# Kernel optimization log

Hardware: AMD Instinct MI355X
Metric: run time of the kernel (lower is better)

The kernel has to match this reference:

```python
import jax, jax.numpy as jnp
import numpy as np
from jax.scipy.special import logsumexp

E = 512      # input_size (= 2*hidden_size)
T = 24       # output_size (num CRF tags)
B, S = 32, 512
HEADS = 2


def setup_inputs() -> dict:
    key = jax.random.key(0)
    ks = jax.random.split(key, 12)
    u = lambda k, shape, a: jax.random.uniform(k, shape, jnp.float32, -a, a)
    inp = {
        "encoder_outputs": jax.random.normal(ks[0], (B, S, E), jnp.float32),
        "labels": jax.random.randint(ks[1], (B, S), 0, T),
        "mask": jnp.ones((B, S), dtype=bool),
        # nn.MultiheadAttention params
        "Win": u(ks[2], (3 * E, E), E ** -0.5),
        "bin_": jnp.zeros((3 * E,), jnp.float32),
        "Wout": u(ks[3], (E, E), E ** -0.5),
        "bout": jnp.zeros((E,), jnp.float32),
        # crf_linear
        "crf_w": u(ks[4], (T, E), E ** -0.5),
        "crf_b": u(ks[5], (T,), E ** -0.5),
        # torchcrf CRF params (uniform(-0.1, 0.1))
        "start_t": u(ks[6], (T,), 0.1),
        "end_t": u(ks[7], (T,), 0.1),
        "trans": u(ks[8], (T, T), 0.1),
        # entity_linear
        "ent_w": u(ks[9], (2, E), E ** -0.5),
        "ent_b": u(ks[10], (2,), E ** -0.5),
    }
    return inp


def _mha(x, Win, bin_, Wout, bout):
    b, s, e = x.shape
    hd = e // HEADS
    qkv = x @ Win.T + bin_                       # [B,S,3E]
    q, k, v = jnp.split(qkv, 3, axis=-1)
    q = q.reshape(b, s, HEADS, hd)
    k = k.reshape(b, s, HEADS, hd)
    v = v.reshape(b, s, HEADS, hd)
    scores = jnp.einsum("bqhd,bkhd->bhqk", q, k) / jnp.sqrt(jnp.float32(hd))
    attn = jax.nn.softmax(scores, axis=-1)       # [B,H,S,S]
    out = jnp.einsum("bhqk,bkhd->bqhd", attn, v).reshape(b, s, e)
    return out @ Wout.T + bout


def _crf_numerator(em, labels, maskf, start_t, end_t, trans):
    # em: [B,S,T] emissions, labels: [B,S] int, maskf: [B,S] float (mask[:,0]==1)
    bidx = jnp.arange(em.shape[0])
    score = start_t[labels[:, 0]] + em[bidx, 0, labels[:, 0]]
    prev, cur = labels[:, :-1], labels[:, 1:]
    em_t = jnp.take_along_axis(em[:, 1:], cur[:, :, None], axis=2)[..., 0]
    score = score + ((trans[prev, cur] + em_t) * maskf[:, 1:]).sum(axis=1)
    seq_ends = maskf.sum(axis=1).astype(jnp.int32) - 1
    last_tags = labels[bidx, seq_ends]
    return score + end_t[last_tags]


def _crf_normalizer(em, maskf, start_t, end_t, trans):
    score0 = start_t + em[:, 0]                  # [B,T]

    def step(score, x):
        e_t, m_t = x                             # [B,T], [B]
        nxt = logsumexp(score[:, :, None] + trans[None] + e_t[:, None, :], axis=1)
        return jnp.where(m_t[:, None] > 0, nxt, score), None

    xs = (em[:, 1:].swapaxes(0, 1), maskf[:, 1:].T)
    score, _ = jax.lax.scan(step, score0, xs)
    return logsumexp(score + end_t, axis=1)


def _viterbi(em, start_t, end_t, trans):
    # decode is called without a mask -> mask of all ones
    score0 = start_t + em[:, 0]                  # [B,T]

    def step(score, e_t):
        nxt = score[:, :, None] + trans[None] + e_t[:, None, :]  # [B,T,T]
        return nxt.max(axis=1), nxt.argmax(axis=1)

    score, history = jax.lax.scan(step, score0, em[:, 1:].swapaxes(0, 1))
    last = jnp.argmax(score + end_t, axis=1)     # [B]

    def back(tag, hist):
        prev = jnp.take_along_axis(hist, tag[:, None], axis=1)[:, 0]
        return prev, prev

    _, prevs = jax.lax.scan(back, last, history, reverse=True)  # [S-1,B]
    return jnp.concatenate([prevs, last[None]], axis=0).T       # [B,S]


def reference(encoder_outputs, labels, mask, Win, bin_, Wout, bout,
              crf_w, crf_b, start_t, end_t, trans, ent_w, ent_b):
    attn = _mha(encoder_outputs, Win, bin_, Wout, bout)
    dec = jax.nn.relu(attn)                      # [B,S,E]
    fc_out = dec @ crf_w.T + crf_b               # [B,S,T]
    maskf = mask.astype(fc_out.dtype)
    num = _crf_numerator(fc_out, labels, maskf, start_t, end_t, trans)
    den = _crf_normalizer(fc_out, maskf, start_t, end_t, trans)
    llh = (num - den).sum() / maskf.sum()        # reduction='token_mean'
    crf_out = _viterbi(fc_out, start_t, end_t, trans)
    seg_out = jax.nn.log_softmax(dec @ ent_w.T + ent_b, axis=2)
    return crf_out, seg_out, -llh
```

## Files before the change

### kernel.cpp

```cpp
#include <hip/hip_runtime.h>

#define BB 32
#define SS 512
#define EE 512
#define NHH 2
#define HDD 256
#define E3 1536
#define NT 24
#define MR (BB*SS)

#define WAVE_BAR() __builtin_amdgcn_wave_barrier()

typedef _Float16 half8  __attribute__((ext_vector_type(8)));
typedef _Float16 half4v __attribute__((ext_vector_type(4)));
typedef float    f32x4  __attribute__((ext_vector_type(4)));

template<int BN>
__global__ __launch_bounds__(256) void mfma_gemm(
    const float* __restrict__ A, int lda, long sAhi, long sAlo, int zA,
    const float* __restrict__ B, int ldb, long sBhi, long sBlo, int zB,
    const float* __restrict__ bias,
    float* __restrict__ C, int ldc, long sChi, long sClo, int zC,
    int K, int relu)
{
    __shared__ __align__(16) _Float16 sAh[8*640];
    __shared__ __align__(16) _Float16 sAl[8*640];
    __shared__ __align__(16) _Float16 sBh[8*640];
    __shared__ __align__(16) _Float16 sBl[8*640];

    const int t = threadIdx.x;
    const int z = blockIdx.z;
    const int za = zA + z, zb = zB + z, zc = zC + z;
    const float* Ab = A + (size_t)(za>>1)*sAhi + (size_t)(za&1)*sAlo
                        + (size_t)blockIdx.y*128*lda;
    const float* Bb = B + (size_t)(zb>>1)*sBhi + (size_t)(zb&1)*sBlo
                        + (BN ? (size_t)blockIdx.x*128
                              : (size_t)blockIdx.x*128*ldb);

    const int wv = t >> 6, lane = t & 63;
    const int wm = wv >> 1, wn = wv & 1;
    const int lm = lane & 15, lq = lane >> 4;

    f32x4 acc[4][4];
#pragma unroll
    for (int i = 0; i < 4; ++i)
#pragma unroll
        for (int j = 0; j < 4; ++j) acc[i][j] = (f32x4){0.f,0.f,0.f,0.f};

    const int r8  = t >> 3;
    const int kc  = (t & 7) * 4;
    const int bnk = (t >> 7) * 16;
    const int bnn = t & 127;

    for (int k0 = 0; k0 < K; k0 += 32) {
        float4 ga[4], gb[4]; float gv[16];
#pragma unroll
        for (int i = 0; i < 4; ++i)
            ga[i] = *(const float4*)(Ab + (size_t)(r8 + 32*i)*lda + k0 + kc);
        if (BN) {
#pragma unroll
            for (int i = 0; i < 16; ++i)
                gv[i] = Bb[(size_t)(k0 + bnk + i)*ldb + bnn];
        } else {
#pragma unroll
            for (int i = 0; i < 4; ++i)
                gb[i] = *(const float4*)(Bb + (size_t)(r8 + 32*i)*ldb + k0 + kc);
        }
        __syncthreads();
#pragma unroll
        for (int i = 0; i < 4; ++i) {
            const int row  = r8 + 32*i;
            const int base = (row >> 4)*640 + (row & 15)*40 + kc;
            float4 a = ga[i];
            _Float16 h0 = (_Float16)a.x, h1 = (_Float16)a.y,
                     h2 = (_Float16)a.z, h3 = (_Float16)a.w;
            _Float16 l0 = (_Float16)(a.x - (float)h0),
                     l1 = (_Float16)(a.y - (float)h1),
                     l2 = (_Float16)(a.z - (float)h2),
                     l3 = (_Float16)(a.w - (float)h3);
            *(half4v*)&sAh[base] = (half4v){h0,h1,h2,h3};
            *(half4v*)&sAl[base] = (half4v){l0,l1,l2,l3};
        }
        if (BN) {
#pragma unroll
            for (int i = 0; i < 16; ++i) {
                const int k = bnk + i;
                float v = gv[i];
                _Float16 h = (_Float16)v;
                _Float16 l = (_Float16)(v - (float)h);
                const int base = (bnn >> 4)*640 + (bnn & 15)*40 + k;
                sBh[base] = h;
                sBl[base] = l;
            }
        } else {
#pragma unroll
            for (int i = 0; i < 4; ++i) {
                const int row  = r8 + 32*i;
                const int base = (row >> 4)*640 + (row & 15)*40 + kc;
                float4 b = gb[i];
                _Float16 h0 = (_Float16)b.x, h1 = (_Float16)b.y,
                         h2 = (_Float16)b.z, h3 = (_Float16)b.w;
                _Float16 l0 = (_Float16)(b.x - (float)h0),
                         l1 = (_Float16)(b.y - (float)h1),
                         l2 = (_Float16)(b.z - (float)h2),
                         l3 = (_Float16)(b.w - (float)h3);
                *(half4v*)&sBh[base] = (half4v){h0,h1,h2,h3};
                *(half4v*)&sBl[base] = (half4v){l0,l1,l2,l3};
            }
        }
        __syncthreads();

        half8 bhf[4], blf[4];
#pragma unroll
        for (int j = 0; j < 4; ++j) {
            const int tb = (wn*4 + j)*640 + lm*40 + lq*8;
            bhf[j] = *(const half8*)&sBh[tb];
            blf[j] = *(const half8*)&sBl[tb];
        }
#pragma unroll
        for (int i = 0; i < 4; ++i) {
            const int ta = (wm*4 + i)*640 + lm*40 + lq*8;
            half8 ah = *(const half8*)&sAh[ta];
            half8 al = *(const half8*)&sAl[ta];
#pragma unroll
            for (int j = 0; j < 4; ++j) {
                acc[i][j] = __builtin_amdgcn_mfma_f32_16x16x32_f16(ah, bhf[j], acc[i][j], 0, 0, 0);
                acc[i][j] = __builtin_amdgcn_mfma_f32_16x16x32_f16(al, bhf[j], acc[i][j], 0, 0, 0);
                acc[i][j] = __builtin_amdgcn_mfma_f32_16x16x32_f16(ah, blf[j], acc[i][j], 0, 0, 0);
            }
        }
    }

    float* Cb = C + (size_t)(zc>>1)*sChi + (size_t)(zc&1)*sClo;
#pragma unroll
    for (int j = 0; j < 4; ++j) {
        const int col = blockIdx.x*128 + (wn*4 + j)*16 + lm;
        const float bj = bias ? bias[col] : 0.f;
#pragma unroll
        for (int i = 0; i < 4; ++i) {
            const int row0 = blockIdx.y*128 + (wm*4 + i)*16 + lq*4;
#pragma unroll
            for (int r = 0; r < 4; ++r) {
                float v = acc[i][j][r] + bj;
                if (relu) v = fmaxf(v, 0.f);
                Cb[(size_t)(row0 + r)*ldc + col] = v;
            }
        }
    }
}

__global__ __launch_bounds__(256) void softmax_rows(float* __restrict__ scores)
{
    const int w    = threadIdx.x >> 6;
    const int lane = threadIdx.x & 63;
    const size_t row = (size_t)blockIdx.x * 4 + w;
    float* p = scores + row * SS + lane * 8;
    float4 v0 = *(float4*)(p);
    float4 v1 = *(float4*)(p + 4);
    const float scale = 0.0625f;
    float m = fmaxf(fmaxf(fmaxf(v0.x, v0.y), fmaxf(v0.z, v0.w)),
                    fmaxf(fmaxf(v1.x, v1.y), fmaxf(v1.z, v1.w)));
#pragma unroll
    for (int off = 32; off >= 1; off >>= 1) m = fmaxf(m, __shfl_xor(m, off));
    v0.x = __expf((v0.x - m) * scale); v0.y = __expf((v0.y - m) * scale);
    v0.z = __expf((v0.z - m) * scale); v0.w = __expf((v0.w - m) * scale);
    v1.x = __expf((v1.x - m) * scale); v1.y = __expf((v1.y - m) * scale);
    v1.z = __expf((v1.z - m) * scale); v1.w = __expf((v1.w - m) * scale);
    float sum = v0.x + v0.y + v0.z + v0.w + v1.x + v1.y + v1.z + v1.w;
#pragma unroll
    for (int off = 32; off >= 1; off >>= 1) sum += __shfl_xor(sum, off);
    float inv = 1.f / sum;
    v0.x *= inv; v0.y *= inv; v0.z *= inv; v0.w *= inv;
    v1.x *= inv; v1.y *= inv; v1.z *= inv; v1.w *= inv;
    *(float4*)(p)     = v0;
    *(float4*)(p + 4) = v1;
}

__global__ __launch_bounds__(192) void fc_crf_kernel(
    const float* __restrict__ dec, const float* __restrict__ W,
    const float* __restrict__ bias, float* __restrict__ out)
{
    __shared__ __align__(16) float Ws[NT][516];
    for (int i = threadIdx.x; i < NT*128; i += 192) {
        int j = i >> 7, c = (i & 127) * 4;
        *(float4*)&Ws[j][c] = *(const float4*)(W + (size_t)j*EE + c);
    }
    __syncthreads();
    const int t = threadIdx.x;
    const int rloc = t / NT;
    const int j = t - rloc * NT;
    const int row = blockIdx.x * 8 + rloc;
    const float4* a = (const float4*)(dec + (size_t)row * EE);
    float acc = 0.f;
#pragma unroll 4
    for (int i = 0; i < 128; ++i) {
        float4 x = a[i];
        float4 y = *(const float4*)&Ws[j][i*4];
        acc += x.x*y.x + x.y*y.y + x.z*y.z + x.w*y.w;
    }
    out[(size_t)row * NT + j] = acc + bias[j];
}

__global__ __launch_bounds__(256) void crf_seg_kernel(
    const float* __restrict__ fc, const int* __restrict__ labels,
    const float* __restrict__ start_t, const float* __restrict__ end_t,
    const float* __restrict__ trans, const float* __restrict__ dec,
    const float* __restrict__ ent_w, const float* __restrict__ ent_b,
    float* __restrict__ num, float* __restrict__ den,
    float* __restrict__ crf_out, float* __restrict__ segout)
{
    __shared__ unsigned char hist[4][(SS-1)*NT];

    const int blk = blockIdx.x;
    if (blk >= 24) {
        const int w    = threadIdx.x >> 6;
        const int lane = threadIdx.x & 63;
        const int row  = (blk - 24) * 4 + w;
        const float4* a  = (const float4*)(dec + (size_t)row * EE);
        const float4* w0 = (const float4*)(ent_w);
        const float4* w1 = (const float4*)(ent_w + EE);
        float acc0 = 0.f, acc1 = 0.f;
#pragma unroll
        for (int i = 0; i < 2; ++i) {
            int idx = lane * 2 + i;
            float4 x = a[idx];
            float4 u = w0[idx];
            float4 v = w1[idx];
            acc0 += x.x*u.x + x.y*u.y + x.z*u.z + x.w*u.w;
            acc1 += x.x*v.x + x.y*v.y + x.z*v.z + x.w*v.w;
        }
#pragma unroll
        for (int off = 32; off >= 1; off >>= 1) {
            acc0 += __shfl_xor(acc0, off);
            acc1 += __shfl_xor(acc1, off);
        }
        if (lane == 0) {
            float l0 = acc0 + ent_b[0];
            float l1 = acc1 + ent_b[1];
            float m  = fmaxf(l0, l1);
            float lse = m + __logf(__expf(l0 - m) + __expf(l1 - m));
            segout[(size_t)row*2 + 0] = l0 - lse;
            segout[(size_t)row*2 + 1] = l1 - lse;
        }
        return;
    }

    const int w    = threadIdx.x >> 6;
    const int lane = threadIdx.x & 63;
    const int task = blk * 4 + w;
    const int role = task >> 5;
    const int b    = task & 31;
    const float* fcb = fc + (size_t)b * SS * NT;

    if (role == 2) {
        float acc = 0.f;
        for (int s = 1 + lane; s < SS; s += 64) {
            int prev = labels[b*SS + s - 1];
            int cur  = labels[b*SS + s];
            acc += trans[prev*NT + cur] + fcb[(size_t)s*NT + cur];
        }
        if (lane == 0) {
            int l0 = labels[b*SS];
            acc += start_t[l0] + fcb[l0] + end_t[labels[b*SS + SS - 1]];
        }
#pragma unroll
        for (int off = 32; off >= 1; off >>= 1) acc += __shfl_xor(acc, off);
        if (lane == 0) num[b] = acc;
        return;
    }

    const int j = (lane < NT) ? lane : 0;
    float trC[NT];
#pragma unroll
    for (int i = 0; i < NT; ++i) trC[i] = trans[i*NT + j];
    float sc = start_t[j] + fcb[j];

    if (role == 0) {
        float em_next = fcb[NT + j];
        for (int s = 1; s < SS; ++s) {
            float em = em_next;
            int snx = (s + 1 < SS) ? s + 1 : s;
            em_next = fcb[(size_t)snx * NT + j];
            float tv[NT];
#pragma unroll
            for (int i = 0; i < NT; ++i) tv[i] = __shfl(sc, i) + trC[i];
            float mx[NT];
#pragma unroll
            for (int i = 0; i < NT; ++i) mx[i] = tv[i];
#pragma unroll
            for (int st = 1; st < NT; st <<= 1)
#pragma unroll
                for (int i = 0; i + st < NT; i += 2*st)
                    mx[i] = fmaxf(mx[i], mx[i+st]);
            const float m = mx[0];
            float ev[NT];
#pragma unroll
            for (int i = 0; i < NT; ++i) ev[i] = __expf(tv[i] - m);
#pragma unroll
            for (int st = 1; st < NT; st <<= 1)
#pragma unroll
                for (int i = 0; i + st < NT; i += 2*st)
                    ev[i] += ev[i+st];
            sc = m + __logf(ev[0]) + em;
        }
        float v = (lane < NT) ? sc + end_t[j] : -1e30f;
        float m2 = v;
#pragma unroll
        for (int off = 32; off >= 1; off >>= 1) m2 = fmaxf(m2, __shfl_xor(m2, off));
        float e = (lane < NT) ? __expf(v - m2) : 0.f;
#pragma unroll
        for (int off = 32; off >= 1; off >>= 1) e += __shfl_xor(e, off);
        if (lane == 0) den[b] = m2 + __logf(e);
    } else {
        volatile unsigned char* hw = hist[w];
        float em_next = fcb[NT + j];
        for (int s = 1; s < SS; ++s) {
            float em = em_next;
            int snx = (s + 1 < SS) ? s + 1 : s;
            em_next = fcb[(size_t)snx * NT + j];
            float tv[NT]; int ti[NT];
#pragma unroll
            for (int i = 0; i < NT; ++i) { tv[i] = __shfl(sc, i) + trC[i]; ti[i] = i; }
#pragma unroll
            for (int st = 1; st < NT; st <<= 1)
#pragma unroll
                for (int i = 0; i + st < NT; i += 2*st)
                    if (tv[i+st] > tv[i]) { tv[i] = tv[i+st]; ti[i] = ti[i+st]; }
            sc = tv[0] + em;
            if (lane < NT) hw[(s-1)*NT + lane] = (unsigned char)ti[0];
        }
        float bv = (lane < NT) ? sc + end_t[j] : -1e30f;
        int bi = (lane < NT) ? lane : NT;
#pragma unroll
        for (int off = 32; off >= 1; off >>= 1) {
            float ov = __shfl_xor(bv, off);
            int   oi = __shfl_xor(bi, off);
            if (ov > bv || (ov == bv && oi < bi)) { bv = ov; bi = oi; }
        }
        WAVE_BAR();
        if (lane == 0) {
            int tag = bi;
            crf_out[(size_t)b*SS + SS - 1] = (float)tag;
            for (int s = SS - 2; s >= 0; --s) {
                tag = hw[s*NT + tag];
                crf_out[(size_t)b*SS + s] = (float)tag;
            }
        }
    }
}

__global__ __launch_bounds__(64) void llh_kernel(
    const float* __restrict__ num, const float* __restrict__ den,
    float* __restrict__ out)
{
    int t = threadIdx.x;
    float v = (t < BB) ? (num[t] - den[t]) : 0.f;
#pragma unroll
    for (int off = 32; off >= 1; off >>= 1) v += __shfl_xor(v, off);
    if (t == 0) out[(size_t)MR * 3] = -(v / (float)MR);
}

extern "C" void kernel_launch(void* const* d_in, const int* in_sizes, int n_in,
                              void* d_out, int out_size, void* d_ws, size_t ws_size,
                              hipStream_t stream) {
    const float* enc     = (const float*)d_in[0];
    const int*   labels  = (const int*)  d_in[1];
    const float* Win     = (const float*)d_in[3];
    const float* bin     = (const float*)d_in[4];
    const float* Wout    = (const float*)d_in[5];
    const float* bout    = (const float*)d_in[6];
    const float* crf_w   = (const float*)d_in[7];
    const float* crf_b   = (const float*)d_in[8];
    const float* start_t = (const float*)d_in[9];
    const float* end_t   = (const float*)d_in[10];
    const float* trans   = (const float*)d_in[11];
    const float* ent_w   = (const float*)d_in[12];
    const float* ent_b   = (const float*)d_in[13];
    float* out = (float*)d_out;

    float* ws   = (float*)d_ws;
    float* qkv  = ws;
    float* attn = qkv  + (size_t)MR * E3;
    float* big  = attn + (size_t)MR * EE;
    float* sch  = big;
    float* dec  = big;
    float* fc   = big  + (size_t)MR * EE;
    float* num  = fc   + (size_t)MR * NT;
    float* den  = num  + BB;

    dim3 blk(256);
    mfma_gemm<0><<<dim3(E3/128, MR/128, 1), blk, 0, stream>>>(
        enc, EE, 0, 0, 0,  Win, EE, 0, 0, 0,  bin,
        qkv, E3, 0, 0, 0,  EE, 0);
    for (int p = 0; p < 2; ++p) {
        int zoff = p * 32;
        mfma_gemm<0><<<dim3(SS/128, SS/128, 32), blk, 0, stream>>>(
            qkv,      E3, (long)SS*E3, HDD, zoff,
            qkv + EE, E3, (long)SS*E3, HDD, zoff,
            nullptr,
            sch, SS, 2L*SS*SS, (long)SS*SS, 0,
            HDD, 0);
        softmax_rows<<<(32*SS)/4, blk, 0, stream>>>(sch);
        mfma_gemm<1><<<dim3(HDD/128, SS/128, 32), blk, 0, stream>>>(
            sch, SS, 2L*SS*SS, (long)SS*SS, 0,
            qkv + 2*EE, E3, (long)SS*E3, HDD, zoff,
            nullptr,
            attn, EE, (long)SS*EE, HDD, zoff,
            SS, 0);
    }
    mfma_gemm<0><<<dim3(EE/128, MR/128, 1), blk, 0, stream>>>(
        attn, EE, 0, 0, 0,  Wout, EE, 0, 0, 0,  bout,
        dec, EE, 0, 0, 0,  EE, 1);
    fc_crf_kernel<<<MR/8, dim3(192), 0, stream>>>(dec, crf_w, crf_b, fc);
    crf_seg_kernel<<<24 + MR/4, blk, 0, stream>>>(
        fc, labels, start_t, end_t, trans, dec, ent_w, ent_b,
        num, den, out, out + MR);
    llh_kernel<<<1, 64, 0, stream>>>(num, den, out);
}
```

Baseline: 653.7 us.

## Use exp-space matvec for CRF forward and one-wave blocks for CRF/seg kernel

The CRF forward recursion now precomputes exp(trans) once per lane and, each step, multiplies broadcast exp(score - max) values against it. This replaces 24 per-step exponentials and a tree reduction with a single exponential plus FMA accumulation. The CRF/segment kernel also moves from 4-wave blocks to single-wave blocks, so each sequential CRF chain runs on its own CU slot and the seg rows get one block each. Precomputing exp(trans) can lose range if transition values were large, and the number of launched blocks grows roughly fourfold.

```diff
diff --git a/kernel.cpp b/kernel.cpp
--- a/kernel.cpp
+++ b/kernel.cpp
@@ -201,7 +201,7 @@
     out[(size_t)row * NT + j] = acc + bias[j];
 }
 
-__global__ __launch_bounds__(256) void crf_seg_kernel(
+__global__ __launch_bounds__(64, 1) void crf_seg_kernel(
     const float* __restrict__ fc, const int* __restrict__ labels,
     const float* __restrict__ start_t, const float* __restrict__ end_t,
     const float* __restrict__ trans, const float* __restrict__ dec,
@@ -209,13 +209,13 @@
     float* __restrict__ num, float* __restrict__ den,
     float* __restrict__ crf_out, float* __restrict__ segout)
 {
-    __shared__ unsigned char hist[4][(SS-1)*NT];
-
-    const int blk = blockIdx.x;
-    if (blk >= 24) {
-        const int w    = threadIdx.x >> 6;
-        const int lane = threadIdx.x & 63;
-        const int row  = (blk - 24) * 4 + w;
+    __shared__ unsigned char hist[(SS-1)*NT];
+
+    const int blk  = blockIdx.x;
+    const int lane = threadIdx.x;
+
+    if (blk >= 96) {
+        const int row = blk - 96;
         const float4* a  = (const float4*)(dec + (size_t)row * EE);
         const float4* w0 = (const float4*)(ent_w);
         const float4* w1 = (const float4*)(ent_w + EE);
@@ -245,11 +245,8 @@
         return;
     }
 
-    const int w    = threadIdx.x >> 6;
-    const int lane = threadIdx.x & 63;
-    const int task = blk * 4 + w;
-    const int role = task >> 5;
-    const int b    = task & 31;
+    const int role = blk >> 5;
+    const int b    = blk & 31;
     const float* fcb = fc + (size_t)b * SS * NT;
 
     if (role == 2) {
@@ -270,38 +267,39 @@
     }
 
     const int j = (lane < NT) ? lane : 0;
-    float trC[NT];
-#pragma unroll
-    for (int i = 0; i < NT; ++i) trC[i] = trans[i*NT + j];
     float sc = start_t[j] + fcb[j];
 
     if (role == 0) {
+        float etr[NT];
+#pragma unroll
+        for (int i = 0; i < NT; ++i) etr[i] = __expf(trans[i*NT + j]);
         float em_next = fcb[NT + j];
         for (int s = 1; s < SS; ++s) {
             float em = em_next;
             int snx = (s + 1 < SS) ? s + 1 : s;
             em_next = fcb[(size_t)snx * NT + j];
-            float tv[NT];
-#pragma unroll
-            for (int i = 0; i < NT; ++i) tv[i] = __shfl(sc, i) + trC[i];
-            float mx[NT];
-#pragma unroll
-            for (int i = 0; i < NT; ++i) mx[i] = tv[i];
+            float sv[NT];
+#pragma unroll
+            for (int i = 0; i < NT; ++i) sv[i] = __shfl(sc, i);
 #pragma unroll
             for (int st = 1; st < NT; st <<= 1)
 #pragma unroll
                 for (int i = 0; i + st < NT; i += 2*st)
-                    mx[i] = fmaxf(mx[i], mx[i+st]);
-            const float m = mx[0];
+                    sv[i] = fmaxf(sv[i], sv[i+st]);
+            const float m = sv[0];
+            const float eo = __expf(sc - m);
             float ev[NT];
 #pragma unroll
-            for (int i = 0; i < NT; ++i) ev[i] = __expf(tv[i] - m);
-#pragma unroll
-            for (int st = 1; st < NT; st <<= 1)
-#pragma unroll
-                for (int i = 0; i + st < NT; i += 2*st)
-                    ev[i] += ev[i+st];
-            sc = m + __logf(ev[0]) + em;
+            for (int i = 0; i < NT; ++i) ev[i] = __shfl(eo, i);
+            float a0 = 0.f, a1 = 0.f, a2 = 0.f, a3 = 0.f;
+#pragma unroll
+            for (int i = 0; i < NT; i += 4) {
+                a0 = fmaf(ev[i+0], etr[i+0], a0);
+                a1 = fmaf(ev[i+1], etr[i+1], a1);
+                a2 = fmaf(ev[i+2], etr[i+2], a2);
+                a3 = fmaf(ev[i+3], etr[i+3], a3);
+            }
+            sc = m + __logf((a0 + a1) + (a2 + a3)) + em;
         }
         float v = (lane < NT) ? sc + end_t[j] : -1e30f;
         float m2 = v;
@@ -312,7 +310,9 @@
         for (int off = 32; off >= 1; off >>= 1) e += __shfl_xor(e, off);
         if (lane == 0) den[b] = m2 + __logf(e);
     } else {
-        volatile unsigned char* hw = hist[w];
+        float trC[NT];
+#pragma unroll
+        for (int i = 0; i < NT; ++i) trC[i] = trans[i*NT + j];
         float em_next = fcb[NT + j];
         for (int s = 1; s < SS; ++s) {
             float em = em_next;
@@ -327,7 +327,7 @@
                 for (int i = 0; i + st < NT; i += 2*st)
                     if (tv[i+st] > tv[i]) { tv[i] = tv[i+st]; ti[i] = ti[i+st]; }
             sc = tv[0] + em;
-            if (lane < NT) hw[(s-1)*NT + lane] = (unsigned char)ti[0];
+            if (lane < NT) hist[(s-1)*NT + lane] = (unsigned char)ti[0];
         }
         float bv = (lane < NT) ? sc + end_t[j] : -1e30f;
         int bi = (lane < NT) ? lane : NT;
@@ -337,12 +337,12 @@
             int   oi = __shfl_xor(bi, off);
             if (ov > bv || (ov == bv && oi < bi)) { bv = ov; bi = oi; }
         }
-        WAVE_BAR();
+        __syncthreads();
         if (lane == 0) {
             int tag = bi;
             crf_out[(size_t)b*SS + SS - 1] = (float)tag;
             for (int s = SS - 2; s >= 0; --s) {
-                tag = hw[s*NT + tag];
+                tag = hist[s*NT + tag];
                 crf_out[(size_t)b*SS + s] = (float)tag;
             }
         }
@@ -412,7 +412,7 @@
         attn, EE, 0, 0, 0,  Wout, EE, 0, 0, 0,  bout,
         dec, EE, 0, 0, 0,  EE, 1);
     fc_crf_kernel<<<MR/8, dim3(192), 0, stream>>>(dec, crf_w, crf_b, fc);
-    crf_seg_kernel<<<24 + MR/4, blk, 0, stream>>>(
+    crf_seg_kernel<<<96 + MR, dim3(64), 0, stream>>>(
         fc, labels, start_t, end_t, trans, dec, ent_w, ent_b,
         num, den, out, out + MR);
     llh_kernel<<<1, 64, 0, stream>>>(num, den, out);
```

New measurement: 606.4 us. 7.2% less time.
